# Optimization experiments

Measured on AMD Instinct MI355X. Metric: run time of the kernel, lower is better.

The kernel has to match this reference:

```python
import jax, jax.numpy as jnp
import numpy as np

TOP_K = 2

def setup_inputs() -> dict:
    key = jax.random.key(0)
    k1, k2, k3, k4 = jax.random.split(key, 4)
    N, H, F, E = 2048, 1024, 2048, 8
    x = jax.random.normal(k1, (N, H), dtype=jnp.float32)
    router_weight = jax.random.normal(k2, (H, E), dtype=jnp.float32) * 0.02
    w1 = jax.random.normal(k3, (E, H, F), dtype=jnp.float32) * 0.02
    w2 = jax.random.normal(k4, (E, F, H), dtype=jnp.float32) * 0.02
    return {"x": x, "router_weight": router_weight, "w1": w1, "w2": w2}

def reference(x, router_weight, w1, w2):
    # Router: softmax over experts, top-k, renormalize (matches torch forward).
    N = x.shape[0]
    E = router_weight.shape[1]
    logits = x.astype(jnp.float32) @ router_weight            # [N, E]
    rprobs = jax.nn.softmax(logits, axis=-1)
    topk_p, topk_i = jax.lax.top_k(rprobs, TOP_K)             # [N, K]
    topk_p = topk_p / jnp.sum(topk_p, axis=-1, keepdims=True)
    # Scatter normalized top-k probs into dense [N, E] gate matrix; zeros
    # everywhere else, so gating subsumes the boolean routing_map.
    probs = jnp.zeros((N, E), dtype=jnp.float32).at[
        jnp.arange(N)[:, None], topk_i].set(topk_p)
    # Expert FFN (same math as permute -> grouped GEMM -> weighted scatter-add:
    # out[t] = sum_e probs[t,e] * gelu(x[t] @ w1[e]) @ w2[e]).
    h = jnp.einsum('nh,ehf->enf', x, w1)                      # [E, N, F]
    h = jax.nn.gelu(h, approximate=False)                     # torch F.gelu is erf-based
    y = jnp.einsum('enf,efh->enh', h, w2)                     # [E, N, H]
    out = jnp.einsum('enh,ne->nh', y, probs.astype(x.dtype))  # weighted combine
    return out
```

## Files before the change

kernel.cpp:

```cpp
#include <hip/hip_runtime.h>
#include <hip/hip_fp16.h>
#include <math.h>

#define NTOK 2048
#define HID  1024
#define FFN  2048
#define NEXP 8

#define BM 128
#define BN 128
#define BK 32
#define LDK 36
#define MAX_TILES 40

#define WS_COUNTS 0
#define WS_SEG    32
#define WS_PROBS  128
#define WS_LISTS  (128 + NTOK*NEXP*4)
#define WS_XH     262144
#define WS_HBUF   (WS_XH + NTOK*HID*2)

typedef _Float16 half8 __attribute__((ext_vector_type(8)));
typedef __fp16   fp16x2 __attribute__((ext_vector_type(2)));
typedef float    f32x4 __attribute__((ext_vector_type(4)));
typedef unsigned long long u64;

static __device__ __forceinline__ unsigned short f2h_bits(float f) {
  union { _Float16 h; unsigned short u; } v;
  v.h = (_Float16)f;
  return v.u;
}
static __device__ __forceinline__ unsigned pack2(float a, float b) {
  return (unsigned)f2h_bits(a) | ((unsigned)f2h_bits(b) << 16);
}
static __device__ __forceinline__ unsigned cvt2(float a, float b) {
  union { fp16x2 h; unsigned u; } t;
  t.h = __builtin_amdgcn_cvt_pkrtz(a, b);
  return t.u;
}

#define GLOAD16(gsrc, ldst) \
  __builtin_amdgcn_global_load_lds( \
      (const __attribute__((address_space(1))) unsigned int*)(gsrc), \
      (__attribute__((address_space(3))) unsigned int*)(ldst), 16, 0, 0)

#define VMCNT0 asm volatile("s_waitcnt vmcnt(0)" ::: "memory")

__global__ __launch_bounds__(256) void moe_prep(
    const float* __restrict__ x, const float* __restrict__ rw,
    unsigned short* __restrict__ xh,
    int* __restrict__ counts, int* __restrict__ lists, float* __restrict__ probs)
{
  const int tid = threadIdx.x;
  const int wid = tid >> 6, lane = tid & 63;
  const int t = blockIdx.x * 4 + wid;

  const float* xr = x + (size_t)t * HID + lane * 16;
  const float4* xp = reinterpret_cast<const float4*>(xr);
  float4 v0 = xp[0], v1 = xp[1], v2 = xp[2], v3 = xp[3];
  float xv[16] = {v0.x,v0.y,v0.z,v0.w, v1.x,v1.y,v1.z,v1.w,
                  v2.x,v2.y,v2.z,v2.w, v3.x,v3.y,v3.z,v3.w};
  float acc[NEXP];
#pragma unroll
  for (int e = 0; e < NEXP; ++e) acc[e] = 0.f;
#pragma unroll
  for (int j = 0; j < 16; ++j) {
    const float4* rp = reinterpret_cast<const float4*>(rw + (size_t)(lane*16 + j) * NEXP);
    float4 a = rp[0], b = rp[1];
    acc[0] += xv[j]*a.x; acc[1] += xv[j]*a.y; acc[2] += xv[j]*a.z; acc[3] += xv[j]*a.w;
    acc[4] += xv[j]*b.x; acc[5] += xv[j]*b.y; acc[6] += xv[j]*b.z; acc[7] += xv[j]*b.w;
  }
#pragma unroll
  for (int off = 32; off > 0; off >>= 1) {
#pragma unroll
    for (int e = 0; e < NEXP; ++e) acc[e] += __shfl_down(acc[e], off);
  }
  unsigned short* xd = xh + (size_t)t * HID + lane * 16;
  *reinterpret_cast<uint4*>(xd) =
      (uint4){pack2(v0.x,v0.y), pack2(v0.z,v0.w), pack2(v1.x,v1.y), pack2(v1.z,v1.w)};
  *reinterpret_cast<uint4*>(xd + 8) =
      (uint4){pack2(v2.x,v2.y), pack2(v2.z,v2.w), pack2(v3.x,v3.y), pack2(v3.z,v3.w)};
  if (lane == 0) {
    float m = acc[0];
#pragma unroll
    for (int e = 1; e < NEXP; ++e) m = fmaxf(m, acc[e]);
    float p[NEXP];
#pragma unroll
    for (int e = 0; e < NEXP; ++e) p[e] = expf(acc[e] - m);
    int i0 = 0;
#pragma unroll
    for (int e = 1; e < NEXP; ++e) if (p[e] > p[i0]) i0 = e;
    int i1 = -1;
#pragma unroll
    for (int e = 0; e < NEXP; ++e) {
      if (e == i0) continue;
      if (i1 < 0 || p[e] > p[i1]) i1 = e;
    }
    const float inv = 1.f / (p[i0] + p[i1]);
    probs[t * NEXP + i0] = p[i0] * inv;
    probs[t * NEXP + i1] = p[i1] * inv;
    int pos0 = atomicAdd(&counts[i0], 1); lists[i0 * NTOK + pos0] = t;
    int pos1 = atomicAdd(&counts[i1], 1); lists[i1 * NTOK + pos1] = t;
  }
}

__global__ void moe_segoff(const int* __restrict__ counts, int* __restrict__ seg) {
  if (threadIdx.x == 0 && blockIdx.x == 0) {
    int run = 0;
    for (int e = 0; e < NEXP; ++e) {
      seg[e] = run;
      run += ((counts[e] + BM - 1) / BM) * BM;
    }
    seg[NEXP] = run;
  }
}

__global__ __launch_bounds__(256) void moe_gemm1(
    const unsigned short* __restrict__ xh, const float* __restrict__ w1,
    const int* __restrict__ counts, const int* __restrict__ seg,
    const int* __restrict__ lists, unsigned short* __restrict__ hbuf)
{
  const int tile = blockIdx.x >> 4;
  const int jcol = blockIdx.x & 15;
  const int rb = tile * BM;
  if (rb >= seg[NEXP]) return;
  int e = 0;
#pragma unroll
  for (int q = 1; q < NEXP; ++q) if (seg[q] <= rb) e = q;
  const int cnt = counts[e];
  const int rloc0 = rb - seg[e];

  __shared__ int tokL[BM];
  __shared__ __align__(16) unsigned short Asm[2][BM*BK];
  __shared__ __align__(16) unsigned short Bsm[2][BN*LDK];

  const int tid = threadIdx.x;
  if (tid < BM) {
    int rl = rloc0 + tid;
    tokL[tid] = (rl < cnt) ? lists[e * NTOK + rl] : 0;
  }
  __syncthreads();

  const int lane = tid & 63;
  const int wid = tid >> 6;
  const int wr = (wid >> 1) * 64;
  const int wc = (wid & 1) * 64;
  const int lr = (lane >> 4) * 4;
  const int lc = lane & 15;
  const int khi = (lane >> 4) * 8;

  const int cw8 = (lane & 3) * 8;
  const int r0 = wid*16 + (lane >> 2);
  const unsigned short* abase[2];
  abase[0] = xh + (size_t)tokL[r0]      * HID + cw8;
  abase[1] = xh + (size_t)tokL[64 + r0] * HID + cw8;

  const int kb = tid >> 5;
  const int fb = tid & 31;
  const float* bbase = w1 + (size_t)e * HID * FFN + (size_t)jcol * BN + fb * 4;

  f32x4 acc[4][4];
#pragma unroll
  for (int m = 0; m < 4; ++m)
#pragma unroll
    for (int n = 0; n < 4; ++n)
      acc[m][n] = (f32x4){0.f, 0.f, 0.f, 0.f};

  f32x4 bld[4];

#define LOADB1(kk) do { \
    _Pragma("unroll") \
    for (int j = 0; j < 4; ++j) \
      bld[j] = *reinterpret_cast<const f32x4*>(bbase + (size_t)((kk) + kb*4 + j) * FFN); \
  } while (0)

#define STAGEA(buf, kk) do { \
    GLOAD16(abase[0] + (kk), &Asm[buf][(wid*64)*8]); \
    GLOAD16(abase[1] + (kk), &Asm[buf][(256 + wid*64)*8]); \
  } while (0)

#define CVTB(buf) do { \
    _Pragma("unroll") \
    for (int i3 = 0; i3 < 4; ++i3) { \
      uint2 wv; \
      wv.x = cvt2(bld[0][i3], bld[1][i3]); \
      wv.y = cvt2(bld[2][i3], bld[3][i3]); \
      *reinterpret_cast<uint2*>(&Bsm[buf][(fb*4 + i3)*LDK + kb*4]) = wv; \
    } } while (0)

  LOADB1(0);
  STAGEA(0, 0);
  int cur = 0;
  for (int kk = 0; kk < HID; kk += BK) {
    CVTB(cur);
    VMCNT0;
    __syncthreads();
    if (kk + BK < HID) {
      LOADB1(kk + BK);
      STAGEA(cur ^ 1, kk + BK);
    }
    half8 af[4], bf[4];
#pragma unroll
    for (int m = 0; m < 4; ++m)
      af[m] = *reinterpret_cast<const half8*>(&Asm[cur][(wr + m*16 + lc)*BK + khi]);
#pragma unroll
    for (int n = 0; n < 4; ++n) {
      union { u64 q[2]; half8 h; } t;
      const unsigned short* bp = &Bsm[cur][(wc + n*16 + lc)*LDK + khi];
      t.q[0] = *reinterpret_cast<const u64*>(bp);
      t.q[1] = *reinterpret_cast<const u64*>(bp + 4);
      bf[n] = t.h;
    }
#pragma unroll
    for (int m = 0; m < 4; ++m)
#pragma unroll
      for (int n = 0; n < 4; ++n)
        acc[m][n] = __builtin_amdgcn_mfma_f32_16x16x32_f16(af[m], bf[n], acc[m][n], 0, 0, 0);
    cur ^= 1;
  }
#undef LOADB1
#undef CVTB

#pragma unroll
  for (int m = 0; m < 4; ++m) {
#pragma unroll
    for (int r = 0; r < 4; ++r) {
      unsigned short* hp = hbuf + (size_t)(rb + wr + m*16 + lr + r) * FFN + jcol*BN + wc + lc;
#pragma unroll
      for (int n = 0; n < 4; ++n) {
        float v = acc[m][n][r];
        float g = 0.5f * v * (1.f + erff(v * 0.70710678118f));
        hp[n*16] = f2h_bits(g);
      }
    }
  }
}

__global__ __launch_bounds__(256) void moe_gemm2(
    const unsigned short* __restrict__ hbuf, const float* __restrict__ w2,
    const int* __restrict__ counts, const int* __restrict__ seg,
    const int* __restrict__ lists, const float* __restrict__ probs,
    float* __restrict__ out)
{
  const int tile = blockIdx.x >> 4;
  const int jcol = (blockIdx.x >> 1) & 7;
  const int ks   = blockIdx.x & 1;
  const int rb = tile * BM;
  if (rb >= seg[NEXP]) return;
  int e = 0;
#pragma unroll
  for (int q = 1; q < NEXP; ++q) if (seg[q] <= rb) e = q;
  const int cnt = counts[e];
  const int rloc0 = rb - seg[e];
  const int k0 = ks * (FFN / 2);
  const int k1 = k0 + (FFN / 2);

  __shared__ int tokL[BM];
  __shared__ float pL[BM];
  __shared__ __align__(16) unsigned short Asm[2][BM*BK];
  __shared__ __align__(16) unsigned short Bsm[2][BN*LDK];

  const int tid = threadIdx.x;
  if (tid < BM) {
    int rl = rloc0 + tid;
    if (rl < cnt) {
      int tk = lists[e * NTOK + rl];
      tokL[tid] = tk;
      pL[tid] = probs[tk * NEXP + e];
    } else { tokL[tid] = 0; pL[tid] = 0.f; }
  }
  __syncthreads();

  const int lane = tid & 63;
  const int wid = tid >> 6;
  const int wr = (wid >> 1) * 64;
  const int wc = (wid & 1) * 64;
  const int lr = (lane >> 4) * 4;
  const int lc = lane & 15;
  const int khi = (lane >> 4) * 8;

  const int cw8 = (lane & 3) * 8;
  const int r0 = wid*16 + (lane >> 2);
  const unsigned short* abase[2];
  abase[0] = hbuf + (size_t)(rb + r0)      * FFN + cw8;
  abase[1] = hbuf + (size_t)(rb + 64 + r0) * FFN + cw8;

  const int kb = tid >> 5;
  const int fb = tid & 31;
  const float* bbase = w2 + (size_t)e * FFN * HID + (size_t)jcol * BN + fb * 4;

  f32x4 acc[4][4];
#pragma unroll
  for (int m = 0; m < 4; ++m)
#pragma unroll
    for (int n = 0; n < 4; ++n)
      acc[m][n] = (f32x4){0.f, 0.f, 0.f, 0.f};

  f32x4 bld[4];

#define LOADB2(kk) do { \
    _Pragma("unroll") \
    for (int j = 0; j < 4; ++j) \
      bld[j] = *reinterpret_cast<const f32x4*>(bbase + (size_t)((kk) + kb*4 + j) * HID); \
  } while (0)

#define CVTB(buf) do { \
    _Pragma("unroll") \
    for (int i3 = 0; i3 < 4; ++i3) { \
      uint2 wv; \
      wv.x = cvt2(bld[0][i3], bld[1][i3]); \
      wv.y = cvt2(bld[2][i3], bld[3][i3]); \
      *reinterpret_cast<uint2*>(&Bsm[buf][(fb*4 + i3)*LDK + kb*4]) = wv; \
    } } while (0)

  LOADB2(k0);
  STAGEA(0, k0);
  int cur = 0;
  for (int kk = k0; kk < k1; kk += BK) {
    CVTB(cur);
    VMCNT0;
    __syncthreads();
    if (kk + BK < k1) {
      LOADB2(kk + BK);
      STAGEA(cur ^ 1, kk + BK);
    }
    half8 af[4], bf[4];
#pragma unroll
    for (int m = 0; m < 4; ++m)
      af[m] = *reinterpret_cast<const half8*>(&Asm[cur][(wr + m*16 + lc)*BK + khi]);
#pragma unroll
    for (int n = 0; n < 4; ++n) {
      union { u64 q[2]; half8 h; } t;
      const unsigned short* bp = &Bsm[cur][(wc + n*16 + lc)*LDK + khi];
      t.q[0] = *reinterpret_cast<const u64*>(bp);
      t.q[1] = *reinterpret_cast<const u64*>(bp + 4);
      bf[n] = t.h;
    }
#pragma unroll
    for (int m = 0; m < 4; ++m)
#pragma unroll
      for (int n = 0; n < 4; ++n)
        acc[m][n] = __builtin_amdgcn_mfma_f32_16x16x32_f16(af[m], bf[n], acc[m][n], 0, 0, 0);
    cur ^= 1;
  }
#undef LOADB2
#undef CVTB
#undef STAGEA

#pragma unroll
  for (int m = 0; m < 4; ++m) {
#pragma unroll
    for (int r = 0; r < 4; ++r) {
      const int lrow = wr + m*16 + lr + r;
      const int rl = rloc0 + lrow;
      if (rl >= cnt) continue;
      const int tok = tokL[lrow];
      const float p = pL[lrow];
      float* op = out + (size_t)tok * HID + jcol*BN + wc + lc;
#pragma unroll
      for (int n = 0; n < 4; ++n)
        atomicAdd(&op[n*16], p * acc[m][n][r]);
    }
  }
}

extern "C" void kernel_launch(void* const* d_in, const int* in_sizes, int n_in,
                              void* d_out, int out_size, void* d_ws, size_t ws_size,
                              hipStream_t stream) {
  const float* x  = (const float*)d_in[0];
  const float* rw = (const float*)d_in[1];
  const float* w1 = (const float*)d_in[2];
  const float* w2 = (const float*)d_in[3];
  float* out = (float*)d_out;

  char* ws = (char*)d_ws;
  int*   counts = (int*)(ws + WS_COUNTS);
  int*   seg    = (int*)(ws + WS_SEG);
  float* probs  = (float*)(ws + WS_PROBS);
  int*   lists  = (int*)(ws + WS_LISTS);
  unsigned short* xh   = (unsigned short*)(ws + WS_XH);
  unsigned short* hbuf = (unsigned short*)(ws + WS_HBUF);

  hipMemsetAsync(ws, 0, 128, stream);
  hipMemsetAsync(d_out, 0, (size_t)NTOK * HID * sizeof(float), stream);

  moe_prep<<<NTOK/4, 256, 0, stream>>>(x, rw, xh, counts, lists, probs);
  moe_segoff<<<1, 64, 0, stream>>>(counts, seg);
  moe_gemm1<<<MAX_TILES * 16, 256, 0, stream>>>(xh, w1, counts, seg, lists, hbuf);
  moe_gemm2<<<MAX_TILES * 8 * 2, 256, 0, stream>>>(hbuf, w2, counts, seg, lists, probs, out);
}
```

Measured before the change: 176.2 us.

## Deepen GEMM prefetch to two stages ahead with partial vmcnt waits

After: 209.4 us. +18.9%, slower.

```diff
diff --git a/kernel.cpp b/kernel.cpp
--- a/kernel.cpp
+++ b/kernel.cpp
@@ -8,7 +8,6 @@
 #define NEXP 8
 
 #define BM 128
-#define BN 128
 #define BK 32
 #define LDK 36
 #define MAX_TILES 40
@@ -31,7 +30,9 @@
   return v.u;
 }
 static __device__ __forceinline__ unsigned pack2(float a, float b) {
-  return (unsigned)f2h_bits(a) | ((unsigned)f2h_bits(b) << 16);
+  union { fp16x2 h; unsigned u; } v;
+  v.h[0] = (__fp16)a; v.h[1] = (__fp16)b;
+  return v.u;
 }
 static __device__ __forceinline__ unsigned cvt2(float a, float b) {
   union { fp16x2 h; unsigned u; } t;
@@ -44,7 +45,8 @@
       (const __attribute__((address_space(1))) unsigned int*)(gsrc), \
       (__attribute__((address_space(3))) unsigned int*)(ldst), 16, 0, 0)
 
-#define VMCNT0 asm volatile("s_waitcnt vmcnt(0)" ::: "memory")
+#define VMC6 asm volatile("s_waitcnt vmcnt(6)" ::: "memory")
+#define VMC0 asm volatile("s_waitcnt vmcnt(0)" ::: "memory")
 
 __global__ __launch_bounds__(256) void moe_prep(
     const float* __restrict__ x, const float* __restrict__ rw,
@@ -131,8 +133,8 @@
   const int rloc0 = rb - seg[e];
 
   __shared__ int tokL[BM];
-  __shared__ __align__(16) unsigned short Asm[2][BM*BK];
-  __shared__ __align__(16) unsigned short Bsm[2][BN*LDK];
+  __shared__ __align__(16) unsigned short Asm[4][BM*BK];
+  __shared__ __align__(16) unsigned short Bsm[2][128*LDK];
 
   const int tid = threadIdx.x;
   if (tid < BM) {
@@ -157,7 +159,7 @@
 
   const int kb = tid >> 5;
   const int fb = tid & 31;
-  const float* bbase = w1 + (size_t)e * HID * FFN + (size_t)jcol * BN + fb * 4;
+  const float* bbase = w1 + (size_t)e * HID * FFN + (size_t)jcol * 128 + fb * 4;
 
   f32x4 acc[4][4];
 #pragma unroll
@@ -166,66 +168,87 @@
     for (int n = 0; n < 4; ++n)
       acc[m][n] = (f32x4){0.f, 0.f, 0.f, 0.f};
 
-  f32x4 bld[4];
-
-#define LOADB1(kk) do { \
+  f32x4 bldX[4], bldY[4];
+
+#define LOADB1(dst, kk) do { \
     _Pragma("unroll") \
     for (int j = 0; j < 4; ++j) \
-      bld[j] = *reinterpret_cast<const f32x4*>(bbase + (size_t)((kk) + kb*4 + j) * FFN); \
-  } while (0)
-
-#define STAGEA(buf, kk) do { \
+      dst[j] = *reinterpret_cast<const f32x4*>(bbase + (size_t)((kk) + kb*4 + j) * FFN); \
+  } while (0)
+
+#define STAGEA1(buf, kk) do { \
     GLOAD16(abase[0] + (kk), &Asm[buf][(wid*64)*8]); \
     GLOAD16(abase[1] + (kk), &Asm[buf][(256 + wid*64)*8]); \
   } while (0)
 
-#define CVTB(buf) do { \
+#define CVTB1(buf, src) do { \
     _Pragma("unroll") \
     for (int i3 = 0; i3 < 4; ++i3) { \
       uint2 wv; \
-      wv.x = cvt2(bld[0][i3], bld[1][i3]); \
-      wv.y = cvt2(bld[2][i3], bld[3][i3]); \
+      wv.x = cvt2(src[0][i3], src[1][i3]); \
+      wv.y = cvt2(src[2][i3], src[3][i3]); \
       *reinterpret_cast<uint2*>(&Bsm[buf][(fb*4 + i3)*LDK + kb*4]) = wv; \
     } } while (0)
 
-  LOADB1(0);
-  STAGEA(0, 0);
-  int cur = 0;
-  for (int kk = 0; kk < HID; kk += BK) {
-    CVTB(cur);
-    VMCNT0;
-    __syncthreads();
-    if (kk + BK < HID) {
-      LOADB1(kk + BK);
-      STAGEA(cur ^ 1, kk + BK);
-    }
-    half8 af[4], bf[4];
-#pragma unroll
-    for (int m = 0; m < 4; ++m)
-      af[m] = *reinterpret_cast<const half8*>(&Asm[cur][(wr + m*16 + lc)*BK + khi]);
-#pragma unroll
-    for (int n = 0; n < 4; ++n) {
-      union { u64 q[2]; half8 h; } t;
-      const unsigned short* bp = &Bsm[cur][(wc + n*16 + lc)*LDK + khi];
-      t.q[0] = *reinterpret_cast<const u64*>(bp);
-      t.q[1] = *reinterpret_cast<const u64*>(bp + 4);
-      bf[n] = t.h;
-    }
-#pragma unroll
-    for (int m = 0; m < 4; ++m)
-#pragma unroll
-      for (int n = 0; n < 4; ++n)
-        acc[m][n] = __builtin_amdgcn_mfma_f32_16x16x32_f16(af[m], bf[n], acc[m][n], 0, 0, 0);
-    cur ^= 1;
+#define COMPUTE1(cA, cB) do { \
+    half8 af[4], bf[4]; \
+    _Pragma("unroll") \
+    for (int m = 0; m < 4; ++m) \
+      af[m] = *reinterpret_cast<const half8*>(&Asm[cA][(wr + m*16 + lc)*BK + khi]); \
+    _Pragma("unroll") \
+    for (int n = 0; n < 4; ++n) { \
+      union { u64 q[2]; half8 h; } t; \
+      const unsigned short* bp = &Bsm[cB][(wc + n*16 + lc)*LDK + khi]; \
+      t.q[0] = *reinterpret_cast<const u64*>(bp); \
+      t.q[1] = *reinterpret_cast<const u64*>(bp + 4); \
+      bf[n] = t.h; \
+    } \
+    _Pragma("unroll") \
+    for (int m = 0; m < 4; ++m) \
+      _Pragma("unroll") \
+      for (int n = 0; n < 4; ++n) \
+        acc[m][n] = __builtin_amdgcn_mfma_f32_16x16x32_f16(af[m], bf[n], acc[m][n], 0, 0, 0); \
+  } while (0)
+
+  LOADB1(bldX, 0);
+  STAGEA1(0, 0);
+  LOADB1(bldY, BK);
+  STAGEA1(1, BK);
+  CVTB1(0, bldX);
+  VMC6;
+  __syncthreads();
+
+  for (int kk0 = 0; kk0 < HID; kk0 += 4*BK) {
+#pragma unroll
+    for (int u = 0; u < 4; ++u) {
+      const int kk = kk0 + u*BK;
+      const int cA = u;
+      const int nA = (u + 2) & 3;
+      const int cB = u & 1;
+      const int nB = cB ^ 1;
+      const bool has2 = (kk + 2*BK < HID);
+      if (has2) {
+        if (u & 1) { LOADB1(bldY, kk + 2*BK); } else { LOADB1(bldX, kk + 2*BK); }
+        STAGEA1(nA, kk + 2*BK);
+      }
+      COMPUTE1(cA, cB);
+      if (kk + BK < HID) {
+        if (u & 1) { CVTB1(nB, bldX); } else { CVTB1(nB, bldY); }
+        if (has2) { VMC6; } else { VMC0; }
+        __syncthreads();
+      }
+    }
   }
 #undef LOADB1
-#undef CVTB
+#undef STAGEA1
+#undef CVTB1
+#undef COMPUTE1
 
 #pragma unroll
   for (int m = 0; m < 4; ++m) {
 #pragma unroll
     for (int r = 0; r < 4; ++r) {
-      unsigned short* hp = hbuf + (size_t)(rb + wr + m*16 + lr + r) * FFN + jcol*BN + wc + lc;
+      unsigned short* hp = hbuf + (size_t)(rb + wr + m*16 + lr + r) * FFN + jcol*128 + wc + lc;
 #pragma unroll
       for (int n = 0; n < 4; ++n) {
         float v = acc[m][n][r];
@@ -257,8 +280,8 @@
 
   __shared__ int tokL[BM];
   __shared__ float pL[BM];
-  __shared__ __align__(16) unsigned short Asm[2][BM*BK];
-  __shared__ __align__(16) unsigned short Bsm[2][BN*LDK];
+  __shared__ __align__(16) unsigned short Asm[4][BM*BK];
+  __shared__ __align__(16) unsigned short Bsm[2][128*LDK];
 
   const int tid = threadIdx.x;
   if (tid < BM) {
@@ -287,7 +310,7 @@
 
   const int kb = tid >> 5;
   const int fb = tid & 31;
-  const float* bbase = w2 + (size_t)e * FFN * HID + (size_t)jcol * BN + fb * 4;
+  const float* bbase = w2 + (size_t)e * FFN * HID + (size_t)jcol * 128 + fb * 4;
 
   f32x4 acc[4][4];
 #pragma unroll
@@ -296,56 +319,81 @@
     for (int n = 0; n < 4; ++n)
       acc[m][n] = (f32x4){0.f, 0.f, 0.f, 0.f};
 
-  f32x4 bld[4];
-
-#define LOADB2(kk) do { \
+  f32x4 bldX[4], bldY[4];
+
+#define LOADB2(dst, kk) do { \
     _Pragma("unroll") \
     for (int j = 0; j < 4; ++j) \
-      bld[j] = *reinterpret_cast<const f32x4*>(bbase + (size_t)((kk) + kb*4 + j) * HID); \
-  } while (0)
-
-#define CVTB(buf) do { \
+      dst[j] = *reinterpret_cast<const f32x4*>(bbase + (size_t)((kk) + kb*4 + j) * HID); \
+  } while (0)
+
+#define STAGEA2(buf, kk) do { \
+    GLOAD16(abase[0] + (kk), &Asm[buf][(wid*64)*8]); \
+    GLOAD16(abase[1] + (kk), &Asm[buf][(256 + wid*64)*8]); \
+  } while (0)
+
+#define CVTB2(buf, src) do { \
     _Pragma("unroll") \
     for (int i3 = 0; i3 < 4; ++i3) { \
       uint2 wv; \
-      wv.x = cvt2(bld[0][i3], bld[1][i3]); \
-      wv.y = cvt2(bld[2][i3], bld[3][i3]); \
+      wv.x = cvt2(src[0][i3], src[1][i3]); \
+      wv.y = cvt2(src[2][i3], src[3][i3]); \
       *reinterpret_cast<uint2*>(&Bsm[buf][(fb*4 + i3)*LDK + kb*4]) = wv; \
     } } while (0)
 
-  LOADB2(k0);
-  STAGEA(0, k0);
-  int cur = 0;
-  for (int kk = k0; kk < k1; kk += BK) {
-    CVTB(cur);
-    VMCNT0;
-    __syncthreads();
-    if (kk + BK < k1) {
-      LOADB2(kk + BK);
-      STAGEA(cur ^ 1, kk + BK);
-    }
-    half8 af[4], bf[4];
-#pragma unroll
-    for (int m = 0; m < 4; ++m)
-      af[m] = *reinterpret_cast<const half8*>(&Asm[cur][(wr + m*16 + lc)*BK + khi]);
-#pragma unroll
-    for (int n = 0; n < 4; ++n) {
-      union { u64 q[2]; half8 h; } t;
-      const unsigned short* bp = &Bsm[cur][(wc + n*16 + lc)*LDK + khi];
-      t.q[0] = *reinterpret_cast<const u64*>(bp);
-      t.q[1] = *reinterpret_cast<const u64*>(bp + 4);
-      bf[n] = t.h;
-    }
-#pragma unroll
-    for (int m = 0; m < 4; ++m)
-#pragma unroll
-      for (int n = 0; n < 4; ++n)
-        acc[m][n] = __builtin_amdgcn_mfma_f32_16x16x32_f16(af[m], bf[n], acc[m][n], 0, 0, 0);
-    cur ^= 1;
+#define COMPUTE2(cA, cB) do { \
+    half8 af[4], bf[4]; \
+    _Pragma("unroll") \
+    for (int m = 0; m < 4; ++m) \
+      af[m] = *reinterpret_cast<const half8*>(&Asm[cA][(wr + m*16 + lc)*BK + khi]); \
+    _Pragma("unroll") \
+    for (int n = 0; n < 4; ++n) { \
+      union { u64 q[2]; half8 h; } t; \
+      const unsigned short* bp = &Bsm[cB][(wc + n*16 + lc)*LDK + khi]; \
+      t.q[0] = *reinterpret_cast<const u64*>(bp); \
+      t.q[1] = *reinterpret_cast<const u64*>(bp + 4); \
+      bf[n] = t.h; \
+    } \
+    _Pragma("unroll") \
+    for (int m = 0; m < 4; ++m) \
+      _Pragma("unroll") \
+      for (int n = 0; n < 4; ++n) \
+        acc[m][n] = __builtin_amdgcn_mfma_f32_16x16x32_f16(af[m], bf[n], acc[m][n], 0, 0, 0); \
+  } while (0)
+
+  LOADB2(bldX, k0);
+  STAGEA2(0, k0);
+  LOADB2(bldY, k0 + BK);
+  STAGEA2(1, k0 + BK);
+  CVTB2(0, bldX);
+  VMC6;
+  __syncthreads();
+
+  for (int kk0 = k0; kk0 < k1; kk0 += 4*BK) {
+#pragma unroll
+    for (int u = 0; u < 4; ++u) {
+      const int kk = kk0 + u*BK;
+      const int cA = u;
+      const int nA = (u + 2) & 3;
+      const int cB = u & 1;
+      const int nB = cB ^ 1;
+      const bool has2 = (kk + 2*BK < k1);
+      if (has2) {
+        if (u & 1) { LOADB2(bldY, kk + 2*BK); } else { LOADB2(bldX, kk + 2*BK); }
+        STAGEA2(nA, kk + 2*BK);
+      }
+      COMPUTE2(cA, cB);
+      if (kk + BK < k1) {
+        if (u & 1) { CVTB2(nB, bldX); } else { CVTB2(nB, bldY); }
+        if (has2) { VMC6; } else { VMC0; }
+        __syncthreads();
+      }
+    }
   }
 #undef LOADB2
-#undef CVTB
-#undef STAGEA
+#undef STAGEA2
+#undef CVTB2
+#undef COMPUTE2
 
 #pragma unroll
   for (int m = 0; m < 4; ++m) {
@@ -356,7 +404,7 @@
       if (rl >= cnt) continue;
       const int tok = tokL[lrow];
       const float p = pL[lrow];
-      float* op = out + (size_t)tok * HID + jcol*BN + wc + lc;
+      float* op = out + (size_t)tok * HID + jcol*128 + wc + lc;
 #pragma unroll
       for (int n = 0; n < 4; ++n)
         atomicAdd(&op[n*16], p * acc[m][n][r]);
```
